# Kernel tuning notes

Measured on AMD Instinct MI355X. Metric: run time of the kernel, lower is better.

The kernel has to match this reference:

```python
import math
import jax, jax.numpy as jnp
import numpy as np

NUM_POS_FEATS = 128
TEMPERATURE = 10000.0
NORMALIZE = True
SCALE = 2.0 * math.pi


def setup_inputs() -> dict:
    key = jax.random.key(0)
    x = jax.random.normal(key, (32, 256, 96, 96), dtype=jnp.float32)
    mask = jnp.zeros((32, 96, 96), dtype=jnp.bool_)  # all pixels valid
    return {"x": x, "mask": mask}


def reference(x, mask):
    F = NUM_POS_FEATS
    not_mask = ~mask
    # Running position indices along H (axis 1) and W (axis 2): [B,H,W]
    y_embed = jnp.cumsum(not_mask.astype(jnp.float32), axis=1)
    x_embed = jnp.cumsum(not_mask.astype(jnp.float32), axis=2)
    if NORMALIZE:
        eps = 1e-6
        y_embed = y_embed / (y_embed[:, -1:, :] + eps) * SCALE
        x_embed = x_embed / (x_embed[:, :, -1:] + eps) * SCALE
    k = jnp.arange(F)
    # dim_t[k] = temperature ** (2*(k//2)/F); even k -> sin, odd k -> cos
    inv_dim_t = TEMPERATURE ** (-2.0 * (k // 2).astype(jnp.float32) / F)  # [F]
    even = (k % 2 == 0)[None, :, None, None]                              # [1,F,1,1]
    ang_y = y_embed[:, None, :, :] * inv_dim_t[None, :, None, None]       # [B,F,H,W]
    ang_x = x_embed[:, None, :, :] * inv_dim_t[None, :, None, None]       # [B,F,H,W]
    pos_y = jnp.where(even, jnp.sin(ang_y), jnp.cos(ang_y))
    pos_x = jnp.where(even, jnp.sin(ang_x), jnp.cos(ang_x))
    return jnp.concatenate([pos_y, pos_x], axis=1).astype(x.dtype)  # [B,2F,H,W]
```

## Files before the change

### kernel.cpp

```cpp
#include <hip/hip_runtime.h>
#include <hip/hip_bf16.h>


#define BATCH 32
#define HH 96
#define WW 96
#define CC 256
#define F_HALF 128

#define LOG2_TEMP 13.287712379549449f
#define TWO_PI 6.2831853071795864769f

__global__ void pes_cumsum_kernel(const unsigned char* __restrict__ mask,
                                  float* __restrict__ yemb,
                                  float* __restrict__ xemb) {
    int tid = blockIdx.x * blockDim.x + threadIdx.x;
    const float eps = 1e-6f;
    if (tid < BATCH * WW) {
        int b = tid / WW, w = tid % WW;
        const unsigned char* m = mask + (size_t)b * HH * WW + w;
        float* o = yemb + (size_t)b * HH * WW + w;
        float s = 0.f;
        float vals[HH];
#pragma unroll
        for (int h = 0; h < HH; ++h) {
            s += (m[h * WW] == 0) ? 1.f : 0.f;
            vals[h] = s;
        }
        float f = TWO_PI / (s + eps);
#pragma unroll
        for (int h = 0; h < HH; ++h) o[h * WW] = vals[h] * f;
    } else if (tid < 2 * BATCH * HH) {
        int t = tid - BATCH * WW;
        int b = t / HH, h = t % HH;
        const unsigned char* m = mask + ((size_t)b * HH + h) * WW;
        float* o = xemb + ((size_t)b * HH + h) * WW;
        float s = 0.f;
        float vals[WW];
#pragma unroll
        for (int w = 0; w < WW; ++w) {
            s += (m[w] == 0) ? 1.f : 0.f;
            vals[w] = s;
        }
        float f = TWO_PI / (s + eps);
#pragma unroll
        for (int w = 0; w < WW; ++w) o[w] = vals[w] * f;
    }
}

#define W4 (WW / 4)
#define TOTAL4 (BATCH * CC * HH * W4)

__global__ void __launch_bounds__(256)
pes_gen_kernel(const float* __restrict__ yemb,
               const float* __restrict__ xemb,
               float* __restrict__ out) {
    int stride = gridDim.x * blockDim.x;
    for (int i = blockIdx.x * blockDim.x + threadIdx.x; i < TOTAL4; i += stride) {
        int w4 = i % W4;
        int t  = i / W4;
        int h  = t % HH; t /= HH;
        int c  = t % CC;
        int b  = t / CC;

        int k = c & (F_HALF - 1);
        int j = k >> 1;
        float inv = exp2f((float)j * (-2.0f / (float)F_HALF) * LOG2_TEMP);

        const float* embbase = (c < F_HALF) ? yemb : xemb;
        const float4 e = *(const float4*)(embbase + ((size_t)b * HH + h) * WW + w4 * 4);

        bool use_sin = (c & 1) == 0;
        float4 r;
        if (use_sin) {
            r.x = __sinf(e.x * inv);
            r.y = __sinf(e.y * inv);
            r.z = __sinf(e.z * inv);
            r.w = __sinf(e.w * inv);
        } else {
            r.x = __cosf(e.x * inv);
            r.y = __cosf(e.y * inv);
            r.z = __cosf(e.z * inv);
            r.w = __cosf(e.w * inv);
        }
        *(float4*)(out + (size_t)i * 4) = r;
    }
}

extern "C" void kernel_launch(void* const* d_in, const int* in_sizes, int n_in,
                              void* d_out, int out_size, void* d_ws, size_t ws_size,
                              hipStream_t stream) {
    const unsigned char* mask = (const unsigned char*)d_in[1];
    float* out = (float*)d_out;

    float* yemb = (float*)d_ws;
    float* xemb = yemb + (size_t)BATCH * HH * WW;

    {
        int threads = 2 * BATCH * HH;
        int block = 256;
        int grid = (threads + block - 1) / block;
        pes_cumsum_kernel<<<grid, block, 0, stream>>>(mask, yemb, xemb);
    }

    {
        int block = 256;
        int grid = 2048;
        pes_gen_kernel<<<grid, block, 0, stream>>>(yemb, xemb, out);
    }
}
```

Measured before the change: 65.44 us.

## Assign one output plane per block and use nontemporal stores

The generation kernel now launches one block per (batch, channel) plane. Per-plane constants (inverse frequency, sin/cos choice, base pointers) are computed once per block, which replaces the grid-stride loop and its per-element div/mod index decoding. The plane loop is fully unrolled over 9 iterations, and output writes use nontemporal stores to avoid polluting the cache with the large streamed output. The cumsum kernel is also rewritten to make two passes over the mask instead of holding 96 running values in a register array, trading an extra mask read for lower register pressure.

```diff
diff --git a/kernel.cpp b/kernel.cpp
--- a/kernel.cpp
+++ b/kernel.cpp
@@ -11,6 +11,8 @@
 #define LOG2_TEMP 13.287712379549449f
 #define TWO_PI 6.2831853071795864769f
 
+typedef float f32x4 __attribute__((ext_vector_type(4)));
+
 __global__ void pes_cumsum_kernel(const unsigned char* __restrict__ mask,
                                   float* __restrict__ yemb,
                                   float* __restrict__ xemb) {
@@ -21,57 +23,54 @@
         const unsigned char* m = mask + (size_t)b * HH * WW + w;
         float* o = yemb + (size_t)b * HH * WW + w;
         float s = 0.f;
-        float vals[HH];
-#pragma unroll
+        for (int h = 0; h < HH; ++h) s += (m[h * WW] == 0) ? 1.f : 0.f;
+        float f = TWO_PI / (s + eps);
+        float cum = 0.f;
         for (int h = 0; h < HH; ++h) {
-            s += (m[h * WW] == 0) ? 1.f : 0.f;
-            vals[h] = s;
+            cum += (m[h * WW] == 0) ? 1.f : 0.f;
+            o[h * WW] = cum * f;
         }
-        float f = TWO_PI / (s + eps);
-#pragma unroll
-        for (int h = 0; h < HH; ++h) o[h * WW] = vals[h] * f;
     } else if (tid < 2 * BATCH * HH) {
         int t = tid - BATCH * WW;
         int b = t / HH, h = t % HH;
         const unsigned char* m = mask + ((size_t)b * HH + h) * WW;
         float* o = xemb + ((size_t)b * HH + h) * WW;
         float s = 0.f;
-        float vals[WW];
-#pragma unroll
+        for (int w = 0; w < WW; ++w) s += (m[w] == 0) ? 1.f : 0.f;
+        float f = TWO_PI / (s + eps);
+        float cum = 0.f;
         for (int w = 0; w < WW; ++w) {
-            s += (m[w] == 0) ? 1.f : 0.f;
-            vals[w] = s;
+            cum += (m[w] == 0) ? 1.f : 0.f;
+            o[w] = cum * f;
         }
-        float f = TWO_PI / (s + eps);
-#pragma unroll
-        for (int w = 0; w < WW; ++w) o[w] = vals[w] * f;
     }
 }
 
-#define W4 (WW / 4)
-#define TOTAL4 (BATCH * CC * HH * W4)
+#define PLANE   (HH * WW)
+#define PLANE4  (PLANE / 4)
+#define ITERS   (PLANE4 / 256)
 
 __global__ void __launch_bounds__(256)
 pes_gen_kernel(const float* __restrict__ yemb,
                const float* __restrict__ xemb,
                float* __restrict__ out) {
-    int stride = gridDim.x * blockDim.x;
-    for (int i = blockIdx.x * blockDim.x + threadIdx.x; i < TOTAL4; i += stride) {
-        int w4 = i % W4;
-        int t  = i / W4;
-        int h  = t % HH; t /= HH;
-        int c  = t % CC;
-        int b  = t / CC;
+    int p = blockIdx.x;
+    int b = p >> 8;
+    int c = p & (CC - 1);
 
-        int k = c & (F_HALF - 1);
-        int j = k >> 1;
-        float inv = exp2f((float)j * (-2.0f / (float)F_HALF) * LOG2_TEMP);
+    int j = (c & (F_HALF - 1)) >> 1;
+    float inv = exp2f((float)j * (-2.0f / (float)F_HALF) * LOG2_TEMP);
+    bool use_sin = (c & 1) == 0;
 
-        const float* embbase = (c < F_HALF) ? yemb : xemb;
-        const float4 e = *(const float4*)(embbase + ((size_t)b * HH + h) * WW + w4 * 4);
+    const f32x4* ep = (const f32x4*)((c < F_HALF ? yemb : xemb) + (size_t)b * PLANE);
+    f32x4* op = (f32x4*)(out + (size_t)p * PLANE);
 
-        bool use_sin = (c & 1) == 0;
-        float4 r;
+    int t = threadIdx.x;
+#pragma unroll
+    for (int it = 0; it < ITERS; ++it) {
+        int idx = t + it * 256;
+        f32x4 e = ep[idx];
+        f32x4 r;
         if (use_sin) {
             r.x = __sinf(e.x * inv);
             r.y = __sinf(e.y * inv);
@@ -83,7 +82,7 @@
             r.z = __cosf(e.z * inv);
             r.w = __cosf(e.w * inv);
         }
-        *(float4*)(out + (size_t)i * 4) = r;
+        __builtin_nontemporal_store(r, op + idx);
     }
 }
 
@@ -94,7 +93,7 @@
     float* out = (float*)d_out;
 
     float* yemb = (float*)d_ws;
-    float* xemb = yemb + (size_t)BATCH * HH * WW;
+    float* xemb = yemb + (size_t)BATCH * PLANE;
 
     {
         int threads = 2 * BATCH * HH;
@@ -103,9 +102,5 @@
         pes_cumsum_kernel<<<grid, block, 0, stream>>>(mask, yemb, xemb);
     }
 
-    {
-        int block = 256;
-        int grid = 2048;
-        pes_gen_kernel<<<grid, block, 0, stream>>>(yemb, xemb, out);
-    }
+    pes_gen_kernel<<<BATCH * CC, 256, 0, stream>>>(yemb, xemb, out);
 }
```

After: 71.12 us. 1.09x slower.
